# Performance work log

Hardware: AMD Instinct MI355X
Metric: run time of the kernel (lower is better)

The kernel has to match this reference:

```python
import jax, jax.numpy as jnp
import numpy as np

NEG_INF = -1e30

def _pool_unpool(x, k):
    # x: [B, C, H, W]. Non-overlapping max pool with window k (floor-mode,
    # matching torch MaxPool2d default), then MaxUnpool: scatter the pooled max
    # back to its argmax location within each window, zeros elsewhere.
    B, C, H, W = x.shape
    Hc, Wc = (H // k) * k, (W // k) * k  # cropped region covered by windows
    xc = x[:, :, :Hc, :Wc]
    # reshape into windows: [B, C, H/k, k, W/k, k] -> [B, C, H/k, W/k, k*k]
    xw = xc.reshape(B, C, Hc // k, k, Wc // k, k).transpose(0, 1, 2, 4, 3, 5)
    xw = xw.reshape(B, C, Hc // k, Wc // k, k * k)
    mx = jnp.max(xw, axis=-1, keepdims=True)
    am = jnp.argmax(xw, axis=-1)  # first max index, matches torch tie-breaking
    onehot = (jnp.arange(k * k) == am[..., None])
    yw = jnp.where(onehot, mx, jnp.zeros_like(mx))
    yc = yw.reshape(B, C, Hc // k, Wc // k, k, k).transpose(0, 1, 2, 4, 3, 5)
    yc = yc.reshape(B, C, Hc, Wc)
    # output_size=size in torch unpool -> pad uncovered border with zeros
    return jnp.pad(yc, ((0, 0), (0, 0), (0, H - Hc), (0, W - Wc)))

def setup_inputs() -> dict:
    key = jax.random.key(0)
    x = jax.random.uniform(key, (16, 1, 1080, 1920), dtype=jnp.float32)
    return {"x": x}

def reference(x):
    k = 3
    x = _pool_unpool(x, k)
    x = _pool_unpool(x, k + 2)
    x = _pool_unpool(x, k + 3)
    return x
```

## Files before the change

### kernel.cpp

```cpp
#include <hip/hip_runtime.h>
#include <stdint.h>


#define IMG_H 1080
#define IMG_W 1920
#define TH 30
#define TW 240
#define LSTRIDE 256
#define NTHREADS 256

#define GPTR(p) ((const __attribute__((address_space(1))) void*)(p))
#define LPTR(p) ((__attribute__((address_space(3))) void*)(p))

template <int K>
__device__ __forceinline__ void stage(float (&v)[30], int cg, int cc) {
    constexpr int NW = 30 / K;
#pragma unroll
    for (int j = 0; j < NW; ++j) {
        float vm = v[j * K];
#pragma unroll
        for (int rr = 1; rr < K; ++rr) vm = fmaxf(vm, v[j * K + rr]);
        float M = vm;
#pragma unroll
        for (int q = 0; q < K; ++q) M = fmaxf(M, __shfl(vm, cg + q, 64));
        unsigned mask = 0u;
#pragma unroll
        for (int rr = 0; rr < K; ++rr)
            mask |= (v[j * K + rr] == M) ? (1u << rr) : 0u;
        unsigned comb = 0u, pre = 0u;
#pragma unroll
        for (int q = 0; q < K; ++q) {
            const unsigned mq = (unsigned)__shfl((int)mask, cg + q, 64);
            comb |= mq;
            pre |= (q < cc) ? mq : 0u;
        }
        const int R = __ffs(comb) - 1;
        const bool win = ((mask >> R) & 1u) != 0u && ((pre >> R) & 1u) == 0u;
#pragma unroll
        for (int rr = 0; rr < K; ++rr)
            v[j * K + rr] = (win && rr == R) ? M : 0.0f;
    }
}

__global__ __launch_bounds__(NTHREADS) void pooling_nms_kernel(
    const float* __restrict__ x, float* __restrict__ out) {
    __shared__ float tile[TH * LSTRIDE];

    const int t = threadIdx.x;
    const int w = t >> 6;
    const int lane = t & 63;
    const int c = (lane < 60) ? lane : 59;

    const size_t base = (size_t)blockIdx.z * (IMG_H * (size_t)IMG_W) +
                        (size_t)(blockIdx.y * TH) * IMG_W + blockIdx.x * TW;
    const float* src = x + base;
    float* dst = out + base;

    if (lane < 60) {
        for (int r = w; r < TH; r += 4)
            __builtin_amdgcn_global_load_lds(
                GPTR(src + (size_t)r * IMG_W + lane * 4),
                LPTR(&tile[r * LSTRIDE + lane * 4]), 16, 0, 0);
    }
    __syncthreads();

    const int colw = 60 * w + c;
    float v[30];
#pragma unroll
    for (int r = 0; r < TH; ++r) v[r] = tile[r * LSTRIDE + colw];

    {
        const int cg = (c / 3) * 3;
        stage<3>(v, cg, c - cg);
    }
    {
        const int cg = (c / 5) * 5;
        stage<5>(v, cg, c - cg);
    }
    {
        const int cg = (c / 6) * 6;
        stage<6>(v, cg, c - cg);
    }

    if (lane < 60) {
#pragma unroll
        for (int r = 0; r < TH; ++r) tile[r * LSTRIDE + colw] = v[r];
    }
    __syncthreads();

    if (lane < 60) {
        for (int r = w; r < TH; r += 4) {
            const float4 val =
                *reinterpret_cast<const float4*>(&tile[r * LSTRIDE + lane * 4]);
            *reinterpret_cast<float4*>(dst + (size_t)r * IMG_W + lane * 4) = val;
        }
    }
}

extern "C" void kernel_launch(void* const* d_in, const int* in_sizes, int n_in,
                              void* d_out, int out_size, void* d_ws, size_t ws_size,
                              hipStream_t stream) {
    const float* x = (const float*)d_in[0];
    float* out = (float*)d_out;
    dim3 grid(IMG_W / TW, IMG_H / TH, 16);
    pooling_nms_kernel<<<grid, NTHREADS, 0, stream>>>(x, out);
}
```

Measured before the change: 233.3 us.

## Switch per-thread column ownership to row segments with LDS exchange of horizontal maxima

Before, each thread held a full 30-row column and combined windows across lanes with shuffles. Now each thread holds a 30-element horizontal segment of one row. It computes horizontal window maxima in registers, writes them to a shared buffer, and after a barrier reads the K rows of its window group to find the winning row and the first-max position. The aim is to replace the many cross-lane shuffles with vectorised LDS traffic. In exchange it adds several __syncthreads barriers, leaves only 240 of 256 threads active, and performs redundant reads of window rows.

```diff
diff --git a/kernel.cpp b/kernel.cpp
--- a/kernel.cpp
+++ b/kernel.cpp
@@ -6,50 +6,79 @@
 #define IMG_W 1920
 #define TH 30
 #define TW 240
-#define LSTRIDE 256
+#define TS 244
+#define HS 96
+#define HB 12
 #define NTHREADS 256
 
 #define GPTR(p) ((const __attribute__((address_space(1))) void*)(p))
 #define LPTR(p) ((__attribute__((address_space(3))) void*)(p))
 
 template <int K>
-__device__ __forceinline__ void stage(float (&v)[30], int cg, int cc) {
-    constexpr int NW = 30 / K;
+__device__ __forceinline__ void stage(float (&v)[30], float* __restrict__ hbuf,
+                                      int r, int b, bool act) {
+    constexpr int NH = 30 / K;
+    constexpr int NG = (NH + 3) / 4;
+    if (act) {
+        float hp[NG * 4];
 #pragma unroll
-    for (int j = 0; j < NW; ++j) {
-        float vm = v[j * K];
+        for (int q = 0; q < NG * 4; ++q) hp[q] = 0.0f;
 #pragma unroll
-        for (int rr = 1; rr < K; ++rr) vm = fmaxf(vm, v[j * K + rr]);
-        float M = vm;
+        for (int j = 0; j < NH; ++j) {
+            float m = v[j * K];
 #pragma unroll
-        for (int q = 0; q < K; ++q) M = fmaxf(M, __shfl(vm, cg + q, 64));
-        unsigned mask = 0u;
+            for (int c = 1; c < K; ++c) m = fmaxf(m, v[j * K + c]);
+            hp[j] = m;
+        }
+        float* w = hbuf + r * HS + b * HB;
 #pragma unroll
-        for (int rr = 0; rr < K; ++rr)
-            mask |= (v[j * K + rr] == M) ? (1u << rr) : 0u;
-        unsigned comb = 0u, pre = 0u;
+        for (int q = 0; q < NG; ++q)
+            *reinterpret_cast<float4*>(w + 4 * q) =
+                *reinterpret_cast<const float4*>(&hp[4 * q]);
+    }
+    __syncthreads();
+    if (act) {
+        const int g = r / K;
+        const int myrr = r - g * K;
+        float best[NH];
+        int frow[NH];
 #pragma unroll
-        for (int q = 0; q < K; ++q) {
-            const unsigned mq = (unsigned)__shfl((int)mask, cg + q, 64);
-            comb |= mq;
-            pre |= (q < cc) ? mq : 0u;
+        for (int j = 0; j < NH; ++j) { best[j] = -1.0f; frow[j] = -1; }
+        const float* vb = hbuf + (g * K) * HS + b * HB;
+#pragma unroll
+        for (int rr = 0; rr < K; ++rr) {
+            float hr[NG * 4];
+#pragma unroll
+            for (int q = 0; q < NG; ++q)
+                *reinterpret_cast<float4*>(&hr[4 * q]) =
+                    *reinterpret_cast<const float4*>(vb + rr * HS + 4 * q);
+#pragma unroll
+            for (int j = 0; j < NH; ++j)
+                if (hr[j] > best[j]) { best[j] = hr[j]; frow[j] = rr; }
         }
-        const int R = __ffs(comb) - 1;
-        const bool win = ((mask >> R) & 1u) != 0u && ((pre >> R) & 1u) == 0u;
 #pragma unroll
-        for (int rr = 0; rr < K; ++rr)
-            v[j * K + rr] = (win && rr == R) ? M : 0.0f;
+        for (int j = 0; j < NH; ++j) {
+            const bool rowwin = (frow[j] == myrr);
+            bool seen = false;
+#pragma unroll
+            for (int c = 0; c < K; ++c) {
+                const int idx = j * K + c;
+                const bool eq = (v[idx] == best[j]);
+                if (!(rowwin && eq && !seen)) v[idx] = 0.0f;
+                seen = seen || eq;
+            }
+        }
     }
 }
 
 __global__ __launch_bounds__(NTHREADS) void pooling_nms_kernel(
     const float* __restrict__ x, float* __restrict__ out) {
-    __shared__ float tile[TH * LSTRIDE];
+    __shared__ float tile[TH * TS];
+    __shared__ float hbuf[TH * HS];
 
     const int t = threadIdx.x;
     const int w = t >> 6;
     const int lane = t & 63;
-    const int c = (lane < 60) ? lane : 59;
 
     const size_t base = (size_t)blockIdx.z * (IMG_H * (size_t)IMG_W) +
                         (size_t)(blockIdx.y * TH) * IMG_W + blockIdx.x * TW;
@@ -60,39 +89,43 @@
         for (int r = w; r < TH; r += 4)
             __builtin_amdgcn_global_load_lds(
                 GPTR(src + (size_t)r * IMG_W + lane * 4),
-                LPTR(&tile[r * LSTRIDE + lane * 4]), 16, 0, 0);
+                LPTR(&tile[r * TS + lane * 4]), 16, 0, 0);
     }
     __syncthreads();
 
-    const int colw = 60 * w + c;
+    const int r = t >> 3;
+    const int b = t & 7;
+    const bool act = r < TH;
+
     float v[30];
+    if (act) {
+        const float* tp = &tile[r * TS + b * 30];
 #pragma unroll
-    for (int r = 0; r < TH; ++r) v[r] = tile[r * LSTRIDE + colw];
-
-    {
-        const int cg = (c / 3) * 3;
-        stage<3>(v, cg, c - cg);
-    }
-    {
-        const int cg = (c / 5) * 5;
-        stage<5>(v, cg, c - cg);
-    }
-    {
-        const int cg = (c / 6) * 6;
-        stage<6>(v, cg, c - cg);
+        for (int k = 0; k < 15; ++k)
+            *reinterpret_cast<float2*>(&v[2 * k]) =
+                *reinterpret_cast<const float2*>(&tp[2 * k]);
     }
 
-    if (lane < 60) {
+    stage<3>(v, hbuf, r, b, act);
+    __syncthreads();
+    stage<5>(v, hbuf, r, b, act);
+    __syncthreads();
+    stage<6>(v, hbuf, r, b, act);
+
+    if (act) {
+        float* tp = &tile[r * TS + b * 30];
 #pragma unroll
-        for (int r = 0; r < TH; ++r) tile[r * LSTRIDE + colw] = v[r];
+        for (int k = 0; k < 15; ++k)
+            *reinterpret_cast<float2*>(&tp[2 * k]) =
+                *reinterpret_cast<const float2*>(&v[2 * k]);
     }
     __syncthreads();
 
     if (lane < 60) {
-        for (int r = w; r < TH; r += 4) {
+        for (int rr = w; rr < TH; rr += 4) {
             const float4 val =
-                *reinterpret_cast<const float4*>(&tile[r * LSTRIDE + lane * 4]);
-            *reinterpret_cast<float4*>(dst + (size_t)r * IMG_W + lane * 4) = val;
+                *reinterpret_cast<const float4*>(&tile[rr * TS + lane * 4]);
+            *reinterpret_cast<float4*>(dst + (size_t)rr * IMG_W + lane * 4) = val;
         }
     }
 }
```

Result: no change. 234.0 us (+0.3%).
